# Kernel optimization log

Measured on AMD Instinct MI355X. Metric: run time of the kernel, lower is better.

Reference implementation:

```python
import jax, jax.numpy as jnp
import numpy as np

BN_EPS = 1e-5
LRELU_SLOPE = 0.2


def setup_inputs() -> dict:
    key = jax.random.key(0)
    ks = jax.random.split(key, 8)
    B, N, D = 32, 2048, 64      # batch, nodes per graph, latent_dim
    E = 1_000_000               # num edges
    H = 128                     # edge_hidden_dim
    Din = 2 * D + 4             # concat(z_src, z_dst, edge_attr)
    z = jax.random.normal(ks[0], (B, N, D), dtype=jnp.float32)
    edge_index = jax.random.randint(ks[1], (2, E), 0, B * N, dtype=jnp.int64)
    edge_attr = jax.random.normal(ks[2], (E, 4), dtype=jnp.float32)
    W1 = jax.random.normal(ks[3], (Din, H), dtype=jnp.float32) * (1.0 / np.sqrt(Din))
    b1 = jnp.zeros((H,), dtype=jnp.float32)
    gamma = jnp.ones((H,), dtype=jnp.float32)
    beta = jnp.zeros((H,), dtype=jnp.float32)
    W2 = jax.random.normal(ks[4], (H, 1), dtype=jnp.float32) * (1.0 / np.sqrt(H))
    b2 = jnp.zeros((1,), dtype=jnp.float32)
    return {"z": z, "edge_attr": edge_attr, "W1": W1, "b1": b1,
            "gamma": gamma, "beta": beta, "W2": W2, "b2": b2,
            "edge_index": edge_index}


def reference(z, edge_attr, W1, b1, gamma, beta, W2, b2, edge_index):
    B, N, D = z.shape
    zf = z.reshape(-1, D)                       # [B*N, D]
    src, dst = edge_index[0], edge_index[1]
    edge_batch = jnp.clip(src // N, 0, B - 1)
    edge_offsets = edge_batch * N               # batch_offsets[edge_batch]
    src_idx = src % N + edge_offsets
    dst_idx = dst % N + edge_offsets
    edge_input = jnp.concatenate([zf[src_idx], zf[dst_idx], edge_attr], axis=1)  # [E, 2D+4]
    h = edge_input @ W1 + b1                    # [E, H]
    # BatchNorm1d (training mode: biased batch stats over edge dim)
    mu = jnp.mean(h, axis=0)
    var = jnp.mean(jnp.square(h - mu), axis=0)
    h = (h - mu) * jax.lax.rsqrt(var + BN_EPS) * gamma + beta
    h = jnp.where(h >= 0, h, LRELU_SLOPE * h)   # LeakyReLU(0.2)
    return h @ W2 + b2                          # [E, 1]
```

## Files before the change

kernel.cpp:

```cpp
#include <hip/hip_runtime.h>

#define E_EDGES   1000000
#define NNODES    2048
#define DLAT      64
#define HCH       128
#define KP        168
#define TILE      64
#define NTILES    (E_EDGES / TILE)
#define NSPREAD   8
#define GRID_GEMM 2048
#define ZVEC      (32 * 2048 * 64 / 4)
#define ZBLK      512

typedef short  shortx8 __attribute__((ext_vector_type(8)));
typedef float  floatx4 __attribute__((ext_vector_type(4)));

__device__ __forceinline__ unsigned short f2bf(float f) {
  union { float f; unsigned int u; } v; v.f = f;
  unsigned int r = (v.u + 0x7fffu + ((v.u >> 16) & 1u)) >> 16;
  return (unsigned short)r;
}

__global__ void k_prep(const float* __restrict__ z, const float* __restrict__ W1,
                       const float* __restrict__ b1,
                       unsigned short* __restrict__ zb, unsigned short* __restrict__ w1t,
                       float* __restrict__ gstats) {
  int bid = blockIdx.x;
  if (bid < ZBLK) {
    const float4* z4 = (const float4*)z;
    ushort4* zb4 = (ushort4*)zb;
    for (int i = bid * 256 + threadIdx.x; i < ZVEC; i += ZBLK * 256) {
      float4 v = z4[i];
      ushort4 o;
      o.x = f2bf(v.x); o.y = f2bf(v.y); o.z = f2bf(v.z); o.w = f2bf(v.w);
      zb4[i] = o;
    }
  } else if (bid == ZBLK) {
    for (int idx = threadIdx.x; idx < 132 * HCH; idx += 256) {
      int k = idx >> 7, n = idx & 127;
      w1t[n * KP + k] = f2bf(W1[idx]);
    }
    for (int idx = threadIdx.x; idx < HCH * (KP - 132); idx += 256) {
      int n = idx / (KP - 132);
      int k = 132 + (idx - n * (KP - 132));
      w1t[n * KP + k] = (k == 132) ? f2bf(b1[n]) : (unsigned short)0;
    }
  } else {
    for (int i = threadIdx.x; i < NSPREAD * 2 * HCH; i += 256) gstats[i] = 0.f;
  }
}

template<bool OUT>
__global__ __launch_bounds__(256, 2)
void k_gemm(const unsigned short* __restrict__ zb,
            const unsigned short* __restrict__ w1t,
            const int* __restrict__ ei,
            const float* __restrict__ attr,
            float* __restrict__ gstats,
            const float* __restrict__ ab,
            const float* __restrict__ W2,
            const float* __restrict__ b2,
            float* __restrict__ out) {
  __shared__ __align__(16) unsigned short A[TILE * KP];
  __shared__ int rows[TILE * 2];
  __shared__ float s_sum[HCH], s_sq[HCH];
  __shared__ float po[TILE];

  const int tid  = threadIdx.x;
  const int lane = tid & 63;
  const int wave = tid >> 6;
  const int l15  = lane & 15;
  const int quad = lane >> 4;
  const int eh   = wave >> 1;
  const int nh   = wave & 1;

  shortx8 bfr[4][5];
#pragma unroll
  for (int nt = 0; nt < 4; ++nt) {
    const unsigned short* bp = w1t + (nh * 64 + nt * 16 + l15) * KP + quad * 8;
#pragma unroll
    for (int kk = 0; kk < 5; ++kk)
      bfr[nt][kk] = *(const shortx8*)(bp + kk * 32);
  }

  float ea[4], ebb[4], ew2[4], b2v = 0.f;
  float ssum[4] = {0.f, 0.f, 0.f, 0.f}, ssq[4] = {0.f, 0.f, 0.f, 0.f};
  if (OUT) {
#pragma unroll
    for (int nt = 0; nt < 4; ++nt) {
      int c = nh * 64 + nt * 16 + l15;
      ea[nt]  = ab[c];
      ebb[nt] = ab[HCH + c];
      ew2[nt] = W2[c];
    }
    b2v = b2[0];
  } else {
    if (tid < HCH) { s_sum[tid] = 0.f; s_sq[tid] = 0.f; }
  }

  for (int tile = blockIdx.x; tile < NTILES; tile += gridDim.x) {
    const int e0 = tile * TILE;
    __syncthreads();
    if (tid < TILE) {
      int s = ei[e0 + tid];
      int d = ei[E_EDGES + e0 + tid];
      rows[tid * 2]     = s;
      rows[tid * 2 + 1] = (s & ~(NNODES - 1)) | (d & (NNODES - 1));
    }
    __syncthreads();
    {
      const int e = tid >> 2, q = tid & 3;
      const int r = rows[e * 2 + (q >> 1)];
      const uint4* src = (const uint4*)(zb + r * DLAT + (q & 1) * 32);
      uint4* dst = (uint4*)(A + e * KP + q * 32);
      dst[0] = src[0]; dst[1] = src[1]; dst[2] = src[2]; dst[3] = src[3];
    }
    if (tid < 64) {
      float4 av = ((const float4*)attr)[e0 + tid];
      ushort4 a0; a0.x = f2bf(av.x); a0.y = f2bf(av.y); a0.z = f2bf(av.z); a0.w = f2bf(av.w);
      *(ushort4*)(A + tid * KP + 128) = a0;
      ushort4 a1; a1.x = f2bf(1.0f); a1.y = 0; a1.z = 0; a1.w = 0;
      *(ushort4*)(A + tid * KP + 132) = a1;
    } else if (tid < 128) {
      int e = tid - 64;
      uint4 zed = {0, 0, 0, 0};
      *(uint4*)(A + e * KP + 136) = zed;
      *(uint4*)(A + e * KP + 144) = zed;
    } else if (tid < 192) {
      int e = tid - 128;
      uint4 zed = {0, 0, 0, 0};
      *(uint4*)(A + e * KP + 152) = zed;
      *(uint4*)(A + e * KP + 160) = zed;
    }
    __syncthreads();

    floatx4 acc[2][4];
#pragma unroll
    for (int mt = 0; mt < 2; ++mt)
#pragma unroll
      for (int nt = 0; nt < 4; ++nt)
        acc[mt][nt] = (floatx4){0.f, 0.f, 0.f, 0.f};

#pragma unroll
    for (int kk = 0; kk < 5; ++kk) {
      shortx8 afr[2];
#pragma unroll
      for (int mt = 0; mt < 2; ++mt)
        afr[mt] = *(const shortx8*)(A + (eh * 32 + mt * 16 + l15) * KP + kk * 32 + quad * 8);
#pragma unroll
      for (int mt = 0; mt < 2; ++mt)
#pragma unroll
        for (int nt = 0; nt < 4; ++nt)
          acc[mt][nt] = __builtin_amdgcn_mfma_f32_16x16x32_bf16(
              afr[mt], bfr[nt][kk], acc[mt][nt], 0, 0, 0);
    }

    if (!OUT) {
#pragma unroll
      for (int nt = 0; nt < 4; ++nt) {
        float s = 0.f, q = 0.f;
#pragma unroll
        for (int mt = 0; mt < 2; ++mt)
#pragma unroll
          for (int r = 0; r < 4; ++r) {
            float h = acc[mt][nt][r];
            s += h; q += h * h;
          }
        ssum[nt] += s; ssq[nt] += q;
      }
    } else {
      float tpart[2][4];
#pragma unroll
      for (int mt = 0; mt < 2; ++mt)
#pragma unroll
        for (int r = 0; r < 4; ++r) {
          float t = 0.f;
#pragma unroll
          for (int nt = 0; nt < 4; ++nt) {
            float h = acc[mt][nt][r];
            float p = ea[nt] * h + ebb[nt];
            p = (p >= 0.f) ? p : 0.2f * p;
            t += p * ew2[nt];
          }
          t += __shfl_xor(t, 1);
          t += __shfl_xor(t, 2);
          t += __shfl_xor(t, 4);
          t += __shfl_xor(t, 8);
          tpart[mt][r] = t;
        }
      if (nh == 1 && l15 == 0) {
#pragma unroll
        for (int mt = 0; mt < 2; ++mt)
#pragma unroll
          for (int r = 0; r < 4; ++r)
            po[eh * 32 + mt * 16 + quad * 4 + r] = tpart[mt][r];
      }
      __syncthreads();
      if (nh == 0 && l15 == 0) {
#pragma unroll
        for (int mt = 0; mt < 2; ++mt)
#pragma unroll
          for (int r = 0; r < 4; ++r) {
            int el = eh * 32 + mt * 16 + quad * 4 + r;
            out[e0 + el] = tpart[mt][r] + po[el] + b2v;
          }
      }
    }
  }

  if (!OUT) {
#pragma unroll
    for (int nt = 0; nt < 4; ++nt) {
      float s = ssum[nt], q = ssq[nt];
      s += __shfl_xor(s, 16); s += __shfl_xor(s, 32);
      q += __shfl_xor(q, 16); q += __shfl_xor(q, 32);
      if (quad == 0) {
        atomicAdd(&s_sum[nh * 64 + nt * 16 + l15], s);
        atomicAdd(&s_sq [nh * 64 + nt * 16 + l15], q);
      }
    }
    __syncthreads();
    float* dstc = gstats + (blockIdx.x & (NSPREAD - 1)) * 2 * HCH;
    if (tid < HCH)          atomicAdd(&dstc[tid], s_sum[tid]);
    else if (tid < 2 * HCH) atomicAdd(&dstc[tid], s_sq[tid - HCH]);
  }
}

__global__ void k_final(const float* __restrict__ gstats,
                        const float* __restrict__ gamma,
                        const float* __restrict__ beta,
                        float* __restrict__ ab) {
  int c = threadIdx.x;
  if (c < HCH) {
    float S = 0.f, Q = 0.f;
    for (int i = 0; i < NSPREAD; ++i) {
      S += gstats[i * 2 * HCH + c];
      Q += gstats[i * 2 * HCH + HCH + c];
    }
    float inv = 1.0f / (float)E_EDGES;
    float mu = S * inv;
    float var = Q * inv - mu * mu;
    float rstd = rsqrtf(var + 1e-5f);
    float a = gamma[c] * rstd;
    ab[c] = a;
    ab[HCH + c] = beta[c] - mu * a;
  }
}

extern "C" void kernel_launch(void* const* d_in, const int* in_sizes, int n_in,
                              void* d_out, int out_size, void* d_ws, size_t ws_size,
                              hipStream_t stream) {
  const float* z     = (const float*)d_in[0];
  const float* attr  = (const float*)d_in[1];
  const float* W1    = (const float*)d_in[2];
  const float* b1    = (const float*)d_in[3];
  const float* gamma = (const float*)d_in[4];
  const float* beta  = (const float*)d_in[5];
  const float* W2    = (const float*)d_in[6];
  const float* b2    = (const float*)d_in[7];
  const int*   ei    = (const int*)d_in[8];
  float* out = (float*)d_out;

  char* ws = (char*)d_ws;
  unsigned short* zb  = (unsigned short*)ws;
  unsigned short* w1t = (unsigned short*)(ws + 8388608);
  float* gstats       = (float*)(ws + 8431616);
  float* ab           = (float*)(ws + 8439808);

  k_prep<<<ZBLK + 2, 256, 0, stream>>>(z, W1, b1, zb, w1t, gstats);
  k_gemm<false><<<GRID_GEMM, 256, 0, stream>>>(zb, w1t, ei, attr, gstats,
                                               nullptr, W2, b2, nullptr);
  k_final<<<1, 128, 0, stream>>>(gstats, gamma, beta, ab);
  k_gemm<true><<<GRID_GEMM, 256, 0, stream>>>(zb, w1t, ei, attr, gstats,
                                              ab, W2, b2, out);
}
```

Measured before the change: 262.4 us.

## Double-buffer edge tiles with async global-to-LDS gathers and index prefetch

Restructures the edge GEMM loop into a software pipeline. The next tile's z rows are gathered straight into a second LDS buffer with global_load_lds, and edge indices are prefetched two tiles ahead, so gather latency overlaps the MFMA work. The row layout changes to a 128-byte XOR-swizzled z region plus a separate attr/bias region. Output writes are deferred one iteration, which drops a barrier per tile. The grid shrinks to 768 persistent blocks at 3 blocks per CU, which adds register pressure and more complex indexing.

Result: slower. 319.6 us (+21.8%).

```diff
diff --git a/kernel.cpp b/kernel.cpp
--- a/kernel.cpp
+++ b/kernel.cpp
@@ -2,23 +2,30 @@
 
 #define E_EDGES   1000000
 #define NNODES    2048
-#define DLAT      64
 #define HCH       128
-#define KP        168
+#define KPW       168
 #define TILE      64
 #define NTILES    (E_EDGES / TILE)
 #define NSPREAD   8
-#define GRID_GEMM 2048
+#define GRID_GEMM 768
 #define ZVEC      (32 * 2048 * 64 / 4)
 #define ZBLK      512
+#define ZREG      16384
+#define AREG      80
+#define BUFB      (ZREG + TILE * AREG)
 
 typedef short  shortx8 __attribute__((ext_vector_type(8)));
 typedef float  floatx4 __attribute__((ext_vector_type(4)));
-
-__device__ __forceinline__ unsigned short f2bf(float f) {
+typedef __attribute__((address_space(1))) const unsigned int GASU;
+typedef __attribute__((address_space(3))) unsigned int LASU;
+
+__device__ __forceinline__ unsigned int f2bf(float f) {
   union { float f; unsigned int u; } v; v.f = f;
-  unsigned int r = (v.u + 0x7fffu + ((v.u >> 16) & 1u)) >> 16;
-  return (unsigned short)r;
+  return (v.u + 0x7fffu + ((v.u >> 16) & 1u)) >> 16;
+}
+
+__device__ __forceinline__ void gather16(const void* gp, void* lp) {
+  __builtin_amdgcn_global_load_lds((GASU*)gp, (LASU*)lp, 16, 0, 0);
 }
 
 __global__ void k_prep(const float* __restrict__ z, const float* __restrict__ W1,
@@ -32,18 +39,19 @@
     for (int i = bid * 256 + threadIdx.x; i < ZVEC; i += ZBLK * 256) {
       float4 v = z4[i];
       ushort4 o;
-      o.x = f2bf(v.x); o.y = f2bf(v.y); o.z = f2bf(v.z); o.w = f2bf(v.w);
+      o.x = (unsigned short)f2bf(v.x); o.y = (unsigned short)f2bf(v.y);
+      o.z = (unsigned short)f2bf(v.z); o.w = (unsigned short)f2bf(v.w);
       zb4[i] = o;
     }
   } else if (bid == ZBLK) {
     for (int idx = threadIdx.x; idx < 132 * HCH; idx += 256) {
       int k = idx >> 7, n = idx & 127;
-      w1t[n * KP + k] = f2bf(W1[idx]);
-    }
-    for (int idx = threadIdx.x; idx < HCH * (KP - 132); idx += 256) {
-      int n = idx / (KP - 132);
-      int k = 132 + (idx - n * (KP - 132));
-      w1t[n * KP + k] = (k == 132) ? f2bf(b1[n]) : (unsigned short)0;
+      w1t[n * KPW + k] = (unsigned short)f2bf(W1[idx]);
+    }
+    for (int idx = threadIdx.x; idx < HCH * (KPW - 132); idx += 256) {
+      int n = idx / (KPW - 132);
+      int k = 132 + (idx - n * (KPW - 132));
+      w1t[n * KPW + k] = (k == 132) ? (unsigned short)f2bf(b1[n]) : (unsigned short)0;
     }
   } else {
     for (int i = threadIdx.x; i < NSPREAD * 2 * HCH; i += 256) gstats[i] = 0.f;
@@ -51,7 +59,7 @@
 }
 
 template<bool OUT>
-__global__ __launch_bounds__(256, 2)
+__global__ __launch_bounds__(256, 3)
 void k_gemm(const unsigned short* __restrict__ zb,
             const unsigned short* __restrict__ w1t,
             const int* __restrict__ ei,
@@ -61,10 +69,9 @@
             const float* __restrict__ W2,
             const float* __restrict__ b2,
             float* __restrict__ out) {
-  __shared__ __align__(16) unsigned short A[TILE * KP];
-  __shared__ int rows[TILE * 2];
+  __shared__ __align__(16) unsigned char Abuf[2][BUFB];
   __shared__ float s_sum[HCH], s_sq[HCH];
-  __shared__ float po[TILE];
+  __shared__ float po[2][TILE];
 
   const int tid  = threadIdx.x;
   const int lane = tid & 63;
@@ -73,11 +80,12 @@
   const int quad = lane >> 4;
   const int eh   = wave >> 1;
   const int nh   = wave & 1;
+  const int bid  = blockIdx.x;
 
   shortx8 bfr[4][5];
 #pragma unroll
   for (int nt = 0; nt < 4; ++nt) {
-    const unsigned short* bp = w1t + (nh * 64 + nt * 16 + l15) * KP + quad * 8;
+    const unsigned short* bp = w1t + (nh * 64 + nt * 16 + l15) * KPW + quad * 8;
 #pragma unroll
     for (int kk = 0; kk < 5; ++kk)
       bfr[nt][kk] = *(const shortx8*)(bp + kk * 32);
@@ -98,41 +106,101 @@
     if (tid < HCH) { s_sum[tid] = 0.f; s_sq[tid] = 0.f; }
   }
 
-  for (int tile = blockIdx.x; tile < NTILES; tile += gridDim.x) {
-    const int e0 = tile * TILE;
-    __syncthreads();
-    if (tid < TILE) {
-      int s = ei[e0 + tid];
-      int d = ei[E_EDGES + e0 + tid];
-      rows[tid * 2]     = s;
-      rows[tid * 2 + 1] = (s & ~(NNODES - 1)) | (d & (NNODES - 1));
-    }
-    __syncthreads();
+  for (int i = tid; i < 2 * TILE * 3; i += 256) {
+    int b = (i >= TILE * 3);
+    int r = i - b * TILE * 3;
+    int e = r / 3, c = 1 + (r - e * 3);
+    *(uint4*)&Abuf[b][ZREG + e * AREG + c * 16] = (uint4){0u, 0u, 0u, 0u};
+  }
+
+  const bool useDst = (l15 >= 8);
+  int coff[4];
+#pragma unroll
+  for (int j = 0; j < 4; ++j)
+    coff[j] = ((l15 & 7) ^ ((j * 4 + quad) & 7)) << 4;
+
+  int offz[5];
+#pragma unroll
+  for (int kk = 0; kk < 4; ++kk)
+    offz[kk] = (eh * 32 + l15) * 256 + ((((kk * 4 + quad) ^ (l15 & 7))) << 4);
+  offz[4] = ZREG + (eh * 32 + l15) * AREG + quad * 16;
+
+  int t = bid;
+  int rowsN[4];
+  {
+    const int e0 = t * TILE;
+#pragma unroll
+    for (int j = 0; j < 4; ++j) {
+      int e = wave * 16 + j * 4 + quad;
+      int s = ei[e0 + e];
+      int d = ei[E_EDGES + e0 + e];
+      rowsN[j] = useDst ? ((s & ~(NNODES - 1)) | (d & (NNODES - 1))) : s;
+    }
+  }
+#pragma unroll
+  for (int j = 0; j < 4; ++j)
+    gather16((const unsigned char*)zb + rowsN[j] * 128 + coff[j],
+             &Abuf[0][wave * 4096 + j * 1024]);
+  float4 av = {0.f, 0.f, 0.f, 0.f};
+  if (tid < TILE) av = ((const float4*)attr)[t * TILE + tid];
+
+  {
+    int t1 = (t + GRID_GEMM < NTILES) ? t + GRID_GEMM : bid;
+    const int e0 = t1 * TILE;
+#pragma unroll
+    for (int j = 0; j < 4; ++j) {
+      int e = wave * 16 + j * 4 + quad;
+      int s = ei[e0 + e];
+      int d = ei[E_EDGES + e0 + e];
+      rowsN[j] = useDst ? ((s & ~(NNODES - 1)) | (d & (NNODES - 1))) : s;
+    }
+  }
+  if (tid < TILE) {
+    uint4 v;
+    v.x = f2bf(av.x) | (f2bf(av.y) << 16);
+    v.y = f2bf(av.z) | (f2bf(av.w) << 16);
+    v.z = 0x3F80u;
+    v.w = 0u;
+    *(uint4*)&Abuf[0][ZREG + tid * AREG] = v;
+  }
+  __syncthreads();
+
+  int pcur = 0;
+  float prevT[2][4];
+  int prevE0 = -1;
+
+  for (; t < NTILES; t += GRID_GEMM) {
+    const int pn  = pcur ^ 1;
+    const int tn  = (t +     GRID_GEMM < NTILES) ? t +     GRID_GEMM : bid;
+    const int tnn = (t + 2 * GRID_GEMM < NTILES) ? t + 2 * GRID_GEMM : bid;
+
+#pragma unroll
+    for (int j = 0; j < 4; ++j)
+      gather16((const unsigned char*)zb + rowsN[j] * 128 + coff[j],
+               &Abuf[pn][wave * 4096 + j * 1024]);
+    float4 avn = {0.f, 0.f, 0.f, 0.f};
+    if (tid < TILE) avn = ((const float4*)attr)[tn * TILE + tid];
+
+    int sN[4], dN[4];
     {
-      const int e = tid >> 2, q = tid & 3;
-      const int r = rows[e * 2 + (q >> 1)];
-      const uint4* src = (const uint4*)(zb + r * DLAT + (q & 1) * 32);
-      uint4* dst = (uint4*)(A + e * KP + q * 32);
-      dst[0] = src[0]; dst[1] = src[1]; dst[2] = src[2]; dst[3] = src[3];
-    }
-    if (tid < 64) {
-      float4 av = ((const float4*)attr)[e0 + tid];
-      ushort4 a0; a0.x = f2bf(av.x); a0.y = f2bf(av.y); a0.z = f2bf(av.z); a0.w = f2bf(av.w);
-      *(ushort4*)(A + tid * KP + 128) = a0;
-      ushort4 a1; a1.x = f2bf(1.0f); a1.y = 0; a1.z = 0; a1.w = 0;
-      *(ushort4*)(A + tid * KP + 132) = a1;
-    } else if (tid < 128) {
-      int e = tid - 64;
-      uint4 zed = {0, 0, 0, 0};
-      *(uint4*)(A + e * KP + 136) = zed;
-      *(uint4*)(A + e * KP + 144) = zed;
-    } else if (tid < 192) {
-      int e = tid - 128;
-      uint4 zed = {0, 0, 0, 0};
-      *(uint4*)(A + e * KP + 152) = zed;
-      *(uint4*)(A + e * KP + 160) = zed;
-    }
-    __syncthreads();
+      const int e0 = tnn * TILE;
+#pragma unroll
+      for (int j = 0; j < 4; ++j) {
+        int e = wave * 16 + j * 4 + quad;
+        sN[j] = ei[e0 + e];
+        dN[j] = ei[E_EDGES + e0 + e];
+      }
+    }
+
+    if (OUT && prevE0 >= 0 && nh == 0 && l15 == 0) {
+#pragma unroll
+      for (int mt = 0; mt < 2; ++mt)
+#pragma unroll
+        for (int r = 0; r < 4; ++r) {
+          int el = eh * 32 + mt * 16 + quad * 4 + r;
+          out[prevE0 + el] = prevT[mt][r] + po[pcur ^ 1][el] + b2v;
+        }
+    }
 
     floatx4 acc[2][4];
 #pragma unroll
@@ -141,18 +209,16 @@
       for (int nt = 0; nt < 4; ++nt)
         acc[mt][nt] = (floatx4){0.f, 0.f, 0.f, 0.f};
 
+    const unsigned char* base = &Abuf[pcur][0];
 #pragma unroll
     for (int kk = 0; kk < 5; ++kk) {
-      shortx8 afr[2];
-#pragma unroll
-      for (int mt = 0; mt < 2; ++mt)
-        afr[mt] = *(const shortx8*)(A + (eh * 32 + mt * 16 + l15) * KP + kk * 32 + quad * 8);
-#pragma unroll
-      for (int mt = 0; mt < 2; ++mt)
-#pragma unroll
-        for (int nt = 0; nt < 4; ++nt)
-          acc[mt][nt] = __builtin_amdgcn_mfma_f32_16x16x32_bf16(
-              afr[mt], bfr[nt][kk], acc[mt][nt], 0, 0, 0);
+      shortx8 afr0 = *(const shortx8*)(base + offz[kk]);
+      shortx8 afr1 = *(const shortx8*)(base + offz[kk] + (kk < 4 ? 4096 : 1280));
+#pragma unroll
+      for (int nt = 0; nt < 4; ++nt) {
+        acc[0][nt] = __builtin_amdgcn_mfma_f32_16x16x32_bf16(afr0, bfr[nt][kk], acc[0][nt], 0, 0, 0);
+        acc[1][nt] = __builtin_amdgcn_mfma_f32_16x16x32_bf16(afr1, bfr[nt][kk], acc[1][nt], 0, 0, 0);
+      }
     }
 
     if (!OUT) {
@@ -174,41 +240,65 @@
       for (int mt = 0; mt < 2; ++mt)
 #pragma unroll
         for (int r = 0; r < 4; ++r) {
-          float t = 0.f;
+          float tv = 0.f;
 #pragma unroll
           for (int nt = 0; nt < 4; ++nt) {
             float h = acc[mt][nt][r];
             float p = ea[nt] * h + ebb[nt];
             p = (p >= 0.f) ? p : 0.2f * p;
-            t += p * ew2[nt];
+            tv += p * ew2[nt];
           }
-          t += __shfl_xor(t, 1);
-          t += __shfl_xor(t, 2);
-          t += __shfl_xor(t, 4);
-          t += __shfl_xor(t, 8);
-          tpart[mt][r] = t;
+          tv += __shfl_xor(tv, 1);
+          tv += __shfl_xor(tv, 2);
+          tv += __shfl_xor(tv, 4);
+          tv += __shfl_xor(tv, 8);
+          tpart[mt][r] = tv;
         }
       if (nh == 1 && l15 == 0) {
 #pragma unroll
         for (int mt = 0; mt < 2; ++mt)
 #pragma unroll
           for (int r = 0; r < 4; ++r)
-            po[eh * 32 + mt * 16 + quad * 4 + r] = tpart[mt][r];
-      }
-      __syncthreads();
-      if (nh == 0 && l15 == 0) {
+            po[pcur][eh * 32 + mt * 16 + quad * 4 + r] = tpart[mt][r];
+      }
+      if (nh == 0) {
 #pragma unroll
         for (int mt = 0; mt < 2; ++mt)
 #pragma unroll
-          for (int r = 0; r < 4; ++r) {
-            int el = eh * 32 + mt * 16 + quad * 4 + r;
-            out[e0 + el] = tpart[mt][r] + po[el] + b2v;
-          }
-      }
-    }
-  }
-
-  if (!OUT) {
+          for (int r = 0; r < 4; ++r)
+            prevT[mt][r] = tpart[mt][r];
+      }
+      prevE0 = t * TILE;
+    }
+
+    if (tid < TILE) {
+      uint4 v;
+      v.x = f2bf(avn.x) | (f2bf(avn.y) << 16);
+      v.y = f2bf(avn.z) | (f2bf(avn.w) << 16);
+      v.z = 0x3F80u;
+      v.w = 0u;
+      *(uint4*)&Abuf[pn][ZREG + tid * AREG] = v;
+    }
+
+#pragma unroll
+    for (int j = 0; j < 4; ++j)
+      rowsN[j] = useDst ? ((sN[j] & ~(NNODES - 1)) | (dN[j] & (NNODES - 1))) : sN[j];
+
+    __syncthreads();
+    pcur ^= 1;
+  }
+
+  if (OUT) {
+    if (prevE0 >= 0 && nh == 0 && l15 == 0) {
+#pragma unroll
+      for (int mt = 0; mt < 2; ++mt)
+#pragma unroll
+        for (int r = 0; r < 4; ++r) {
+          int el = eh * 32 + mt * 16 + quad * 4 + r;
+          out[prevE0 + el] = prevT[mt][r] + po[pcur ^ 1][el] + b2v;
+        }
+    }
+  } else {
 #pragma unroll
     for (int nt = 0; nt < 4; ++nt) {
       float s = ssum[nt], q = ssq[nt];
@@ -220,7 +310,7 @@
       }
     }
     __syncthreads();
-    float* dstc = gstats + (blockIdx.x & (NSPREAD - 1)) * 2 * HCH;
+    float* dstc = gstats + (bid & (NSPREAD - 1)) * 2 * HCH;
     if (tid < HCH)          atomicAdd(&dstc[tid], s_sum[tid]);
     else if (tid < 2 * HCH) atomicAdd(&dstc[tid], s_sq[tid - HCH]);
   }
```
